# Kernel optimization log

Measured on AMD Instinct MI355X. Metric: run time of the kernel, lower is better.

## Reference

```python
import jax, jax.numpy as jnp
import numpy as np

B, S, D, H, NL, V = 2, 512, 768, 12, 6, 32000
HD = D // H
EPS = 1e-6
# Faithful to original buffer: tril(ones, diagonal=-1) -> True strictly below diagonal,
# and masked_fill sets those to -inf (so each query attends to keys k >= q, as in the source).
MASK = jnp.tril(jnp.ones((S, S), dtype=bool), k=-1)


def setup_inputs() -> dict:
    key = jax.random.key(0)
    ks = jax.random.split(key, 12)
    sc = 0.02
    n = lambda k, shp: jax.random.normal(k, shp, dtype=jnp.float32) * sc
    return {
        "x": jax.random.randint(ks[0], (B, S), 0, V),
        "token_emb": n(ks[1], (V, D)),
        "pos_emb": n(ks[2], (S, D)),
        "norm1_s": jnp.ones((NL, D)), "norm1_b": jnp.zeros((NL, D)),
        "norm2_s": jnp.ones((NL, D)), "norm2_b": jnp.zeros((NL, D)),
        "wq": n(ks[3], (NL, D, D)), "wk": n(ks[4], (NL, D, D)), "wv": n(ks[5], (NL, D, D)),
        "wo": n(ks[6], (NL, D, D)), "bo": jnp.zeros((NL, D)),
        "w1": n(ks[7], (NL, D, 4 * D)), "b1": jnp.zeros((NL, 4 * D)),
        "w2": n(ks[8], (NL, 4 * D, D)), "b2": jnp.zeros((NL, D)),
        "final_s": jnp.ones((D,)), "final_b": jnp.zeros((D,)),
        "head_w": n(ks[9], (D, V)), "head_b": jnp.zeros((V,)),
    }


def _norm(x, s, b):
    # DummyNorm: torch.std default is unbiased (ddof=1); divides by (std + eps), no sqrt(var+eps)
    mean = x.mean(axis=-1, keepdims=True)
    std = jnp.std(x, axis=-1, ddof=1, keepdims=True)
    return s * (x - mean) / (std + EPS) + b


def _gelu(x):
    return 0.5 * x * (1.0 + jnp.tanh(jnp.sqrt(2.0 / jnp.pi) * (x + 0.044715 * x ** 3)))


def _block(x, p):
    wq, wk, wv, wo, bo, w1, b1, w2, b2, n1s, n1b, n2s, n2b = p
    res = x
    h = _norm(x, n1s, n1b)
    q = jnp.einsum("bsd,de->bse", h, wq).reshape(B, S, H, HD)
    k = jnp.einsum("bsd,de->bse", h, wk).reshape(B, S, H, HD)
    v = jnp.einsum("bsd,de->bse", h, wv).reshape(B, S, H, HD)
    scores = jnp.einsum("bqhd,bkhd->bhqk", q, k)
    scores = jnp.where(MASK, -jnp.inf, scores)
    w = jax.nn.softmax(scores / jnp.float32(HD) ** 0.5, axis=-1)  # dropout: eval mode (identity)
    ctx = jnp.einsum("bhqk,bkhd->bqhd", w, v).reshape(B, S, D)
    x = res + (ctx @ wo + bo)
    res = x
    h = _norm(x, n2s, n2b)
    x = res + (_gelu(h @ w1 + b1) @ w2 + b2)
    return x


def reference(x, token_emb, pos_emb, norm1_s, norm1_b, norm2_s, norm2_b,
              wq, wk, wv, wo, bo, w1, b1, w2, b2, final_s, final_b, head_w, head_b):
    h = token_emb[x] + pos_emb[None, :S, :]  # dropout is identity in eval
    params = (wq, wk, wv, wo, bo, w1, b1, w2, b2, norm1_s, norm1_b, norm2_s, norm2_b)
    h = jax.lax.scan(lambda c, p: (_block(c, p), None), h, params)[0]
    h = _norm(h, final_s, final_b)
    return h @ head_w + head_b  # [B, S, V]
```

## Files before the change

### kernel.cpp

```cpp
#include <hip/hip_runtime.h>
#include <math.h>

#define BDIM 2
#define SEQ 512
#define DMODEL 768
#define NHEAD 12
#define HDIM 64
#define NLAYER 6
#define VOCAB 32000
#define MROWS (BDIM*SEQ)
#define EPSV 1e-6f

typedef unsigned short u16;
typedef unsigned int u32;
typedef __bf16 bf16x8 __attribute__((ext_vector_type(8)));
typedef float f32x4 __attribute__((ext_vector_type(4)));

__device__ __forceinline__ u16 f2bf(float f) {
    union { float f; u32 u; } v; v.f = f;
    u32 r = v.u + 0x7fffu + ((v.u >> 16) & 1u);
    return (u16)(r >> 16);
}
__device__ __forceinline__ float bf2f(u16 b) {
    union { u32 u; float f; } v; v.u = ((u32)b) << 16;
    return v.f;
}

__device__ __forceinline__ void gload16(const u16* g, u16* l) {
    __builtin_amdgcn_global_load_lds(
        (const __attribute__((address_space(1))) unsigned int*)g,
        (__attribute__((address_space(3))) unsigned int*)l,
        16, 0, 0);
}

__global__ void embed_kernel(const int* __restrict__ x, const float* __restrict__ tok,
                             const float* __restrict__ pos, float* __restrict__ h) {
    int i = blockIdx.x * blockDim.x + threadIdx.x;
    if (i >= MROWS * DMODEL) return;
    int bs = i / DMODEL, d = i - bs * DMODEL;
    int s = bs & (SEQ - 1);
    h[i] = tok[(size_t)x[bs] * DMODEL + d] + pos[(size_t)s * DMODEL + d];
}

__global__ __launch_bounds__(256) void transpose_conv(const float* __restrict__ in, u16* __restrict__ out,
                                                      int K, int N, long in_bs, long out_bs) {
    __shared__ float t[32][33];
    int b = blockIdx.z;
    int n0 = blockIdx.x * 32, k0 = blockIdx.y * 32;
    int tx = threadIdx.x, ty = threadIdx.y;
    const float* ip = in + (size_t)b * in_bs;
    #pragma unroll
    for (int i = 0; i < 4; ++i)
        t[ty + 8 * i][tx] = ip[(size_t)(k0 + ty + 8 * i) * N + n0 + tx];
    __syncthreads();
    u16* op = out + (size_t)b * out_bs;
    #pragma unroll
    for (int i = 0; i < 4; ++i)
        op[(size_t)(n0 + ty + 8 * i) * K + k0 + tx] = f2bf(t[tx][ty + 8 * i]);
}

template<bool OUTBF>
__global__ __launch_bounds__(256) void norm_kernel(const float* __restrict__ in,
                                                   const float* __restrict__ scale,
                                                   const float* __restrict__ bias,
                                                   void* __restrict__ outp) {
    int row = blockIdx.x;
    const float* xr = in + (size_t)row * DMODEL;
    int t = threadIdx.x;
    float v0 = xr[t], v1 = xr[t + 256], v2 = xr[t + 512];

    float s = v0 + v1 + v2;
    for (int o = 32; o > 0; o >>= 1) s += __shfl_down(s, o);
    __shared__ float red1[4];
    __shared__ float red2[4];
    int wid = t >> 6, lane = t & 63;
    if (lane == 0) red1[wid] = s;
    __syncthreads();
    float mean = (red1[0] + red1[1] + red1[2] + red1[3]) * (1.0f / DMODEL);

    float d0 = v0 - mean, d1 = v1 - mean, d2 = v2 - mean;
    float ss = d0 * d0 + d1 * d1 + d2 * d2;
    for (int o = 32; o > 0; o >>= 1) ss += __shfl_xor(ss, o);
    if (lane == 0) red2[wid] = ss;
    __syncthreads();
    float var = (red2[0] + red2[1] + red2[2] + red2[3]) * (1.0f / (DMODEL - 1));
    float inv = 1.0f / (sqrtf(var) + EPSV);

    size_t o0 = (size_t)row * DMODEL + t;
    float r0 = scale[t] * d0 * inv + bias[t];
    float r1 = scale[t + 256] * d1 * inv + bias[t + 256];
    float r2 = scale[t + 512] * d2 * inv + bias[t + 512];
    if (OUTBF) {
        u16* out = (u16*)outp;
        out[o0] = f2bf(r0); out[o0 + 256] = f2bf(r1); out[o0 + 512] = f2bf(r2);
    } else {
        float* out = (float*)outp;
        out[o0] = r0; out[o0 + 256] = r1; out[o0 + 512] = r2;
    }
}


template<bool OUTBF, bool BIAS, bool RES, bool GELU, bool SWZ>
__global__ __launch_bounds__(256) void gemm_bf16(const u16* __restrict__ A,
                                                 const u16* __restrict__ Wt,
                                                 const float* __restrict__ bias,
                                                 const float* __restrict__ res,
                                                 void* __restrict__ Cout,
                                                 int M, int N, int K) {
    __shared__ u16 Alds[2][128 * 64];
    __shared__ u16 Blds[2][128 * 64];
    int tid = threadIdx.x;
    int lane = tid & 63;
    int wid = tid >> 6;
    int l15 = lane & 15, lk = lane >> 4;
    int wm = (wid >> 1) * 64, wn = (wid & 1) * 64;
    int bm, bn;
    if (SWZ) {
        int id = blockIdx.x;
        int xcd = id & 7, j = id >> 3;
        int g = xcd * ((int)gridDim.x >> 3) + j;
        int mb = M >> 7;
        bn = (g / mb) * 128;
        bm = (g % mb) * 128;
    } else {
        bm = blockIdx.y * 128; bn = blockIdx.x * 128;
    }

    f32x4 acc[4][4];
    #pragma unroll
    for (int i = 0; i < 4; ++i)
        #pragma unroll
        for (int j = 0; j < 4; ++j) { f32x4 z = {0.f, 0.f, 0.f, 0.f}; acc[i][j] = z; }

    int lr  = lane >> 3;
    int lc8 = (lane & 7) ^ lr;
    const u16* gA = A  + (size_t)(bm + lr) * K + lc8 * 8;
    const u16* gB = Wt + (size_t)(bn + lr) * K + lc8 * 8;
    int wrow = wid * 32;

    auto STAGE = [&](int buf, int k0) {
        #pragma unroll
        for (int i = 0; i < 4; ++i) {
            int rb = wrow + i * 8;
            gload16(gA + (size_t)rb * K + k0, &Alds[buf][rb * 64]);
            gload16(gB + (size_t)rb * K + k0, &Blds[buf][rb * 64]);
        }
    };

    STAGE(0, 0);
    __syncthreads();
    int nt = K >> 6;
    int cur = 0;
    for (int t = 0; t < nt; ++t) {
        if (t + 1 < nt) STAGE(cur ^ 1, (t + 1) << 6);

        #pragma unroll
        for (int s = 0; s < 2; ++s) {
            bf16x8 af[4], bfv[4];
            #pragma unroll
            for (int mi = 0; mi < 4; ++mi) {
                int R = wm + mi * 16 + l15;
                af[mi] = *(const bf16x8*)&Alds[cur][R * 64 + (((s * 4 + lk) ^ (R & 7)) << 3)];
            }
            #pragma unroll
            for (int ni = 0; ni < 4; ++ni) {
                int R = wn + ni * 16 + l15;
                bfv[ni] = *(const bf16x8*)&Blds[cur][R * 64 + (((s * 4 + lk) ^ (R & 7)) << 3)];
            }
            #pragma unroll
            for (int mi = 0; mi < 4; ++mi)
                #pragma unroll
                for (int ni = 0; ni < 4; ++ni)
                    acc[mi][ni] = __builtin_amdgcn_mfma_f32_16x16x32_bf16(af[mi], bfv[ni], acc[mi][ni], 0, 0, 0);
        }
        __syncthreads();
        cur ^= 1;
    }

    #pragma unroll
    for (int mi = 0; mi < 4; ++mi) {
        int row0 = bm + wm + mi * 16 + lk * 4;
        #pragma unroll
        for (int ni = 0; ni < 4; ++ni) {
            int col = bn + wn + ni * 16 + l15;
            float bv = BIAS ? bias[col] : 0.0f;
            #pragma unroll
            for (int rr = 0; rr < 4; ++rr) {
                int row = row0 + rr;
                float v = acc[mi][ni][rr] + bv;
                if (GELU) {
                    float xg = v;
                    v = 0.5f * xg * (1.0f + tanhf(0.7978845608028654f * (xg + 0.044715f * xg * xg * xg)));
                }
                if (RES) v += res[(size_t)row * N + col];
                if (OUTBF) ((u16*)Cout)[(size_t)row * N + col] = f2bf(v);
                else       ((float*)Cout)[(size_t)row * N + col] = v;
            }
        }
    }
}

template<bool OUTBF, bool BIAS, bool RES, bool GELU, int BM, int BN>
__global__ __launch_bounds__(256) void gemm_sm(const u16* __restrict__ A,
                                               const u16* __restrict__ Wt,
                                               const float* __restrict__ bias,
                                               const float* __restrict__ res,
                                               void* __restrict__ Cout,
                                               int M, int N, int K) {
    __shared__ u16 Alds[2][BM * 64];
    __shared__ u16 Blds[2][BN * 64];
    int tid = threadIdx.x;
    int lane = tid & 63;
    int wid = tid >> 6;
    int l15 = lane & 15, lk = lane >> 4;
    int wr = wid >> 1, wc = wid & 1;
    int bm = blockIdx.y * BM, bn = blockIdx.x * BN;
    constexpr int MI = BM / 32;
    constexpr int NI = BN / 32;

    f32x4 acc[MI][NI];
    #pragma unroll
    for (int i = 0; i < MI; ++i)
        #pragma unroll
        for (int j = 0; j < NI; ++j) { f32x4 z = {0.f, 0.f, 0.f, 0.f}; acc[i][j] = z; }

    int lr  = lane >> 3;
    int lc8 = (lane & 7) ^ lr;
    const u16* gA = A  + (size_t)(bm + lr) * K + lc8 * 8;
    const u16* gB = Wt + (size_t)(bn + lr) * K + lc8 * 8;

    auto STAGE = [&](int buf, int k0) {
        #pragma unroll
        for (int i = 0; i < MI; ++i) {
            int rb = wid * (BM / 4) + i * 8;
            gload16(gA + (size_t)rb * K + k0, &Alds[buf][rb * 64]);
        }
        #pragma unroll
        for (int i = 0; i < NI; ++i) {
            int rb = wid * (BN / 4) + i * 8;
            gload16(gB + (size_t)rb * K + k0, &Blds[buf][rb * 64]);
        }
    };

    STAGE(0, 0);
    __syncthreads();
    int nt = K >> 6;
    int cur = 0;
    for (int t = 0; t < nt; ++t) {
        if (t + 1 < nt) STAGE(cur ^ 1, (t + 1) << 6);

        #pragma unroll
        for (int s = 0; s < 2; ++s) {
            bf16x8 af[MI], bfv[NI];
            #pragma unroll
            for (int mi = 0; mi < MI; ++mi) {
                int R = wr * (BM / 2) + mi * 16 + l15;
                af[mi] = *(const bf16x8*)&Alds[cur][R * 64 + (((s * 4 + lk) ^ (R & 7)) << 3)];
            }
            #pragma unroll
            for (int ni = 0; ni < NI; ++ni) {
                int R = wc * (BN / 2) + ni * 16 + l15;
                bfv[ni] = *(const bf16x8*)&Blds[cur][R * 64 + (((s * 4 + lk) ^ (R & 7)) << 3)];
            }
            #pragma unroll
            for (int mi = 0; mi < MI; ++mi)
                #pragma unroll
                for (int ni = 0; ni < NI; ++ni)
                    acc[mi][ni] = __builtin_amdgcn_mfma_f32_16x16x32_bf16(af[mi], bfv[ni], acc[mi][ni], 0, 0, 0);
        }
        __syncthreads();
        cur ^= 1;
    }

    #pragma unroll
    for (int mi = 0; mi < MI; ++mi) {
        int row0 = bm + wr * (BM / 2) + mi * 16 + lk * 4;
        #pragma unroll
        for (int ni = 0; ni < NI; ++ni) {
            int col = bn + wc * (BN / 2) + ni * 16 + l15;
            float bv = BIAS ? bias[col] : 0.0f;
            #pragma unroll
            for (int rr = 0; rr < 4; ++rr) {
                int row = row0 + rr;
                float v = acc[mi][ni][rr] + bv;
                if (GELU) {
                    float xg = v;
                    v = 0.5f * xg * (1.0f + tanhf(0.7978845608028654f * (xg + 0.044715f * xg * xg * xg)));
                }
                if (RES) v += res[(size_t)row * N + col];
                if (OUTBF) ((u16*)Cout)[(size_t)row * N + col] = f2bf(v);
                else       ((float*)Cout)[(size_t)row * N + col] = v;
            }
        }
    }
}

__device__ __forceinline__ float bcast_q(float f0, float f1, float f2, float f3, int l15) {
    int src = (l15 >> 2) * 16;
    float a = __shfl(f0, src, 64);
    float b = __shfl(f1, src, 64);
    float c = __shfl(f2, src, 64);
    float d = __shfl(f3, src, 64);
    int r = l15 & 3;
    return r == 0 ? a : (r == 1 ? b : (r == 2 ? c : d));
}

__global__ __launch_bounds__(256) void attn_mfma(const u16* __restrict__ qkv, u16* __restrict__ ctx) {
    int qt = blockIdx.x;
    int bh = blockIdx.y;
    int b = bh / NHEAD, h = bh % NHEAD;
    int tid = threadIdx.x;
    int w = tid >> 6, lane = tid & 63;
    int l15 = lane & 15, lk = lane >> 4;

    __shared__ u16 Klds[64][72];
    __shared__ u16 Vt[64][72];
    __shared__ u16 Plds[4][16][72];

    int q0 = qt * 64;
    const u16* qbase = qkv + (size_t)(b * SEQ + q0 + w * 16 + l15) * 2304 + h * HDIM;
    bf16x8 qf0 = *(const bf16x8*)(qbase + lk * 8);
    bf16x8 qf1 = *(const bf16x8*)(qbase + 32 + lk * 8);

    f32x4 acc_o[4];
    #pragma unroll
    for (int i = 0; i < 4; ++i) { f32x4 z = {0.f,0.f,0.f,0.f}; acc_o[i] = z; }
    float m_run[4] = {-INFINITY, -INFINITY, -INFINITY, -INFINITY};
    float l_run[4] = {0.f, 0.f, 0.f, 0.f};

    int srow = tid >> 2, sc = (tid & 3) * 16;
    int vcol = srow ^ ((sc >> 4) << 4);
    const u16* kg = qkv + (size_t)(b * SEQ) * 2304 + 768  + h * HDIM;
    const u16* vg = qkv + (size_t)(b * SEQ) * 2304 + 1536 + h * HDIM;

    for (int kt = qt; kt < SEQ / 64; ++kt) {
        int kk0 = kt * 64;
        const u16* kp = kg + (size_t)(kk0 + srow) * 2304 + sc;
        const u16* vp = vg + (size_t)(kk0 + srow) * 2304 + sc;
        uint4 kv0 = *(const uint4*)kp, kv1 = *(const uint4*)(kp + 8);
        uint4 vv0 = *(const uint4*)vp, vv1 = *(const uint4*)(vp + 8);
        __syncthreads();
        *(uint4*)&Klds[srow][sc]     = kv0;
        *(uint4*)&Klds[srow][sc + 8] = kv1;
        {
            const u16* vs = (const u16*)&vv0;
            #pragma unroll
            for (int i = 0; i < 8; ++i) Vt[sc + i][vcol] = vs[i];
            const u16* vs1 = (const u16*)&vv1;
            #pragma unroll
            for (int i = 0; i < 8; ++i) Vt[sc + 8 + i][vcol] = vs1[i];
        }
        __syncthreads();

        f32x4 accs[4];
        #pragma unroll
        for (int kb = 0; kb < 4; ++kb) { f32x4 z = {0.f,0.f,0.f,0.f}; accs[kb] = z; }
        __builtin_amdgcn_s_setprio(1);
        #pragma unroll
        for (int kb = 0; kb < 4; ++kb) {
            bf16x8 kf0 = *(const bf16x8*)&Klds[kb * 16 + l15][lk * 8];
            bf16x8 kf1 = *(const bf16x8*)&Klds[kb * 16 + l15][32 + lk * 8];
            accs[kb] = __builtin_amdgcn_mfma_f32_16x16x32_bf16(qf0, kf0, accs[kb], 0, 0, 0);
            accs[kb] = __builtin_amdgcn_mfma_f32_16x16x32_bf16(qf1, kf1, accs[kb], 0, 0, 0);
        }
        __builtin_amdgcn_s_setprio(0);

        bool diag = (kt == qt);
        float s[4][4];
        #pragma unroll
        for (int kb = 0; kb < 4; ++kb)
            #pragma unroll
            for (int r = 0; r < 4; ++r) {
                float v = accs[kb][r] * 0.125f;
                if (diag && (kk0 + kb * 16 + l15) < (q0 + w * 16 + lk * 4 + r)) v = -INFINITY;
                s[kb][r] = v;
            }
        float fac[4];
        #pragma unroll
        for (int r = 0; r < 4; ++r) {
            float mx = fmaxf(fmaxf(s[0][r], s[1][r]), fmaxf(s[2][r], s[3][r]));
            #pragma unroll
            for (int o = 8; o >= 1; o >>= 1) mx = fmaxf(mx, __shfl_xor(mx, o, 64));
            float mn = fmaxf(m_run[r], mx);
            fac[r] = expf(m_run[r] - mn);
            m_run[r] = mn;
        }
        u16 pb[4][4];
        #pragma unroll
        for (int r = 0; r < 4; ++r) {
            float rs = 0.f;
            #pragma unroll
            for (int kb = 0; kb < 4; ++kb) {
                float p = expf(s[kb][r] - m_run[r]);
                pb[kb][r] = f2bf(p);
                rs += p;
            }
            #pragma unroll
            for (int o = 8; o >= 1; o >>= 1) rs += __shfl_xor(rs, o, 64);
            l_run[r] = l_run[r] * fac[r] + rs;
        }
        #pragma unroll
        for (int kb = 0; kb < 4; ++kb)
            #pragma unroll
            for (int r = 0; r < 4; ++r)
                Plds[w][lk * 4 + r][kb * 16 + l15] = pb[kb][r];
        float fq = bcast_q(fac[0], fac[1], fac[2], fac[3], l15);
        #pragma unroll
        for (int db = 0; db < 4; ++db)
            #pragma unroll
            for (int r = 0; r < 4; ++r) acc_o[db][r] *= fq;
        __syncthreads();

        __builtin_amdgcn_s_setprio(1);
        #pragma unroll
        for (int ks = 0; ks < 2; ++ks) {
            bf16x8 pf = *(const bf16x8*)&Plds[w][l15][ks * 32 + lk * 8];
            #pragma unroll
            for (int db = 0; db < 4; ++db) {
                bf16x8 vf = *(const bf16x8*)&Vt[db * 16 + l15][(ks * 32 + lk * 8) ^ (db << 4)];
                acc_o[db] = __builtin_amdgcn_mfma_f32_16x16x32_bf16(vf, pf, acc_o[db], 0, 0, 0);
            }
        }
        __builtin_amdgcn_s_setprio(0);
    }

    float invq;
    {
        float i0 = 1.0f / l_run[0], i1 = 1.0f / l_run[1], i2 = 1.0f / l_run[2], i3 = 1.0f / l_run[3];
        invq = bcast_q(i0, i1, i2, i3, l15);
    }
    u16* cp = ctx + (size_t)(b * SEQ + q0 + w * 16 + l15) * DMODEL + h * HDIM;
    #pragma unroll
    for (int db = 0; db < 4; ++db) {
        ushort4 st;
        st.x = f2bf(acc_o[db][0] * invq);
        st.y = f2bf(acc_o[db][1] * invq);
        st.z = f2bf(acc_o[db][2] * invq);
        st.w = f2bf(acc_o[db][3] * invq);
        *(ushort4*)(cp + db * 16 + lk * 4) = st;
    }
}

template<bool BIAS, bool RES, bool GELU>
__global__ __launch_bounds__(256) void gemm_f32(const float* __restrict__ A, const float* __restrict__ W,
                                                const float* __restrict__ bias, const float* __restrict__ res,
                                                float* __restrict__ C, int M, int N, int K) {
    const int BM = 64, BN = 64, BK = 16;
    __shared__ float sA[BK][BM + 4];
    __shared__ float sB[BK][BN + 4];
    int tid = threadIdx.x;
    int tx = tid & 15, ty = tid >> 4;
    int bm = blockIdx.y * BM, bn = blockIdx.x * BN;
    float acc[4][4] = {};
    const float* Ab = A + (size_t)bm * K;
    const float* Wb = W + bn;
    for (int k0 = 0; k0 < K; k0 += BK) {
        {
            int rr = tid >> 2, c = (tid & 3) * 4;
            float4 va = *(const float4*)(Ab + (size_t)rr * K + k0 + c);
            sA[c + 0][rr] = va.x; sA[c + 1][rr] = va.y; sA[c + 2][rr] = va.z; sA[c + 3][rr] = va.w;
        }
        {
            int rr = tid >> 4, c = (tid & 15) * 4;
            float4 vb = *(const float4*)(Wb + (size_t)(k0 + rr) * N + c);
            *(float4*)(&sB[rr][c]) = vb;
        }
        __syncthreads();
        #pragma unroll
        for (int kk = 0; kk < BK; ++kk) {
            float4 a4 = *(const float4*)(&sA[kk][ty * 4]);
            float4 b4 = *(const float4*)(&sB[kk][tx * 4]);
            float a[4] = {a4.x, a4.y, a4.z, a4.w};
            float b[4] = {b4.x, b4.y, b4.z, b4.w};
            #pragma unroll
            for (int i = 0; i < 4; ++i)
                #pragma unroll
                for (int j = 0; j < 4; ++j) acc[i][j] += a[i] * b[j];
        }
        __syncthreads();
    }
    #pragma unroll
    for (int i = 0; i < 4; ++i) {
        int row = bm + ty * 4 + i;
        #pragma unroll
        for (int j = 0; j < 4; ++j) {
            int col = bn + tx * 4 + j;
            float v = acc[i][j];
            if (BIAS) v += bias[col];
            if (GELU) { float xg = v; v = 0.5f * xg * (1.0f + tanhf(0.7978845608028654f * (xg + 0.044715f * xg * xg * xg))); }
            if (RES) v += res[(size_t)row * N + col];
            C[(size_t)row * N + col] = v;
        }
    }
}

__global__ __launch_bounds__(256) void attn_f32(const float* __restrict__ q, const float* __restrict__ k,
                                                const float* __restrict__ v, float* __restrict__ ctx) {
    int blk = blockIdx.x;
    int qi = blk & (SEQ - 1);
    int tmp = blk >> 9;
    int h = tmp % NHEAD;
    int b = tmp / NHEAD;
    int tid = threadIdx.x;
    __shared__ float qv[HDIM];
    __shared__ float p[SEQ];
    __shared__ float rmax[4];
    __shared__ float rsum[4];
    __shared__ float part[4][HDIM];
    const float* qptr = q + ((size_t)(b * SEQ + qi) * DMODEL + h * HDIM);
    if (tid < HDIM) qv[tid] = qptr[tid];
    __syncthreads();
    float sc[2];
    #pragma unroll
    for (int c = 0; c < 2; ++c) {
        int kk = tid + c * 256;
        const float* kptr = k + ((size_t)(b * SEQ + kk) * DMODEL + h * HDIM);
        float dot = 0.0f;
        #pragma unroll
        for (int d = 0; d < HDIM; ++d) dot += qv[d] * kptr[d];
        sc[c] = (kk >= qi) ? dot * 0.125f : -INFINITY;
    }
    int wid = tid >> 6, lane = tid & 63;
    float m = fmaxf(sc[0], sc[1]);
    for (int o = 32; o > 0; o >>= 1) m = fmaxf(m, __shfl_down(m, o));
    if (lane == 0) rmax[wid] = m;
    __syncthreads();
    m = fmaxf(fmaxf(rmax[0], rmax[1]), fmaxf(rmax[2], rmax[3]));
    float e0 = expf(sc[0] - m);
    float e1 = expf(sc[1] - m);
    p[tid] = e0; p[tid + 256] = e1;
    float sum = e0 + e1;
    for (int o = 32; o > 0; o >>= 1) sum += __shfl_down(sum, o);
    if (lane == 0) rsum[wid] = sum;
    __syncthreads();
    float inv = 1.0f / (rsum[0] + rsum[1] + rsum[2] + rsum[3]);
    int d = tid & 63, ch = tid >> 6;
    float accv = 0.0f;
    const float* vbase = v + ((size_t)b * SEQ * DMODEL + h * HDIM + d);
    for (int kk = ch * 128; kk < (ch + 1) * 128; ++kk) accv += p[kk] * vbase[(size_t)kk * DMODEL];
    part[ch][d] = accv;
    __syncthreads();
    if (tid < HDIM) {
        float rv = (part[0][tid] + part[1][tid] + part[2][tid] + part[3][tid]) * inv;
        ctx[((size_t)(b * SEQ + qi) * DMODEL + h * HDIM + tid)] = rv;
    }
}

extern "C" void kernel_launch(void* const* d_in, const int* in_sizes, int n_in,
                              void* d_out, int out_size, void* d_ws, size_t ws_size,
                              hipStream_t stream) {
    const int*   x   = (const int*)d_in[0];
    const float* tok = (const float*)d_in[1];
    const float* pos = (const float*)d_in[2];
    const float* n1s = (const float*)d_in[3];
    const float* n1b = (const float*)d_in[4];
    const float* n2s = (const float*)d_in[5];
    const float* n2b = (const float*)d_in[6];
    const float* wq  = (const float*)d_in[7];
    const float* wk  = (const float*)d_in[8];
    const float* wv  = (const float*)d_in[9];
    const float* wo  = (const float*)d_in[10];
    const float* bo  = (const float*)d_in[11];
    const float* w1  = (const float*)d_in[12];
    const float* b1  = (const float*)d_in[13];
    const float* w2  = (const float*)d_in[14];
    const float* b2  = (const float*)d_in[15];
    const float* fs  = (const float*)d_in[16];
    const float* fb  = (const float*)d_in[17];
    const float* hw  = (const float*)d_in[18];
    const float* hb  = (const float*)d_in[19];
    float* out = (float*)d_out;

    const size_t szWtQKV = (size_t)NLAYER * 2304 * 768 * 2;
    const size_t szWtO   = (size_t)NLAYER * 768 * 768 * 2;
    const size_t szWt1   = (size_t)NLAYER * 3072 * 768 * 2;
    const size_t szWt2   = (size_t)NLAYER * 768 * 3072 * 2;
    const size_t szWtH   = (size_t)VOCAB * 768 * 2;
    const size_t szH     = (size_t)MROWS * DMODEL * 4;
    const size_t szHN    = (size_t)MROWS * DMODEL * 2;
    const size_t szQKV   = (size_t)MROWS * 2304 * 2;
    const size_t szCTX   = (size_t)MROWS * DMODEL * 2;
    const size_t szFF    = (size_t)MROWS * 3072 * 2;
    const size_t NEED = szWtQKV + szWtO + szWt1 + szWt2 + szWtH + szH + szHN + szQKV + szCTX + szFF;

    if (ws_size >= NEED) {
        char* p = (char*)d_ws;
        u16* WtQKV = (u16*)p; p += szWtQKV;
        u16* WtO   = (u16*)p; p += szWtO;
        u16* Wt1   = (u16*)p; p += szWt1;
        u16* Wt2   = (u16*)p; p += szWt2;
        u16* WtH   = (u16*)p; p += szWtH;
        float* h   = (float*)p; p += szH;
        u16* hn    = (u16*)p; p += szHN;
        u16* qkv   = (u16*)p; p += szQKV;
        u16* ctx   = (u16*)p; p += szCTX;
        u16* ff    = (u16*)p; p += szFF;

        dim3 tb(32, 8);
        transpose_conv<<<dim3(24, 24, NLAYER), tb, 0, stream>>>(wq, WtQKV + 0 * 768 * 768, 768, 768, 768 * 768, 2304 * 768);
        transpose_conv<<<dim3(24, 24, NLAYER), tb, 0, stream>>>(wk, WtQKV + 1 * 768 * 768, 768, 768, 768 * 768, 2304 * 768);
        transpose_conv<<<dim3(24, 24, NLAYER), tb, 0, stream>>>(wv, WtQKV + 2 * 768 * 768, 768, 768, 768 * 768, 2304 * 768);
        transpose_conv<<<dim3(24, 24, NLAYER), tb, 0, stream>>>(wo, WtO, 768, 768, 768 * 768, 768 * 768);
        transpose_conv<<<dim3(96, 24, NLAYER), tb, 0, stream>>>(w1, Wt1, 768, 3072, 768 * 3072, 3072 * 768);
        transpose_conv<<<dim3(24, 96, NLAYER), tb, 0, stream>>>(w2, Wt2, 3072, 768, 3072 * 768, 768 * 3072);
        transpose_conv<<<dim3(1000, 24, 1), tb, 0, stream>>>(hw, WtH, 768, VOCAB, 0, 0);

        embed_kernel<<<(MROWS * DMODEL + 255) / 256, 256, 0, stream>>>(x, tok, pos, h);

        for (int l = 0; l < NLAYER; ++l) {
            const u16* wtqkv = WtQKV + (size_t)l * 2304 * 768;
            const u16* wto   = WtO   + (size_t)l * 768 * 768;
            const u16* wt1   = Wt1   + (size_t)l * 3072 * 768;
            const u16* wt2   = Wt2   + (size_t)l * 768 * 3072;

            norm_kernel<true><<<MROWS, 256, 0, stream>>>(h, n1s + l * DMODEL, n1b + l * DMODEL, hn);
            gemm_sm<true,false,false,false,64,64><<<dim3(36, 16), 256, 0, stream>>>(hn, wtqkv, nullptr, nullptr, qkv, MROWS, 2304, 768);
            attn_mfma<<<dim3(8, 24), 256, 0, stream>>>(qkv, ctx);
            gemm_sm<false,true,true,false,32,64><<<dim3(12, 32), 256, 0, stream>>>(ctx, wto, bo + l * DMODEL, h, h, MROWS, 768, 768);
            norm_kernel<true><<<MROWS, 256, 0, stream>>>(h, n2s + l * DMODEL, n2b + l * DMODEL, hn);
            gemm_sm<true,true,false,true,64,64><<<dim3(48, 16), 256, 0, stream>>>(hn, wt1, b1 + (size_t)l * 3072, nullptr, ff, MROWS, 3072, 768);
            gemm_sm<false,true,true,false,32,64><<<dim3(12, 32), 256, 0, stream>>>(ff, wt2, b2 + l * DMODEL, h, h, MROWS, 768, 3072);
        }
        norm_kernel<true><<<MROWS, 256, 0, stream>>>(h, fs, fb, hn);
        gemm_bf16<false,true,false,false,true><<<2000, 256, 0, stream>>>(hn, WtH, hb, nullptr, out, MROWS, VOCAB, 768);
        return;
    }

    float* ws  = (float*)d_ws;
    float* h   = ws;
    float* hnf = h   + (size_t)MROWS * DMODEL;
    float* qb  = hnf + (size_t)MROWS * DMODEL;
    float* kb  = qb  + (size_t)MROWS * DMODEL;
    float* vb  = kb  + (size_t)MROWS * DMODEL;
    float* ctxf= vb  + (size_t)MROWS * DMODEL;
    float* fff = ctxf+ (size_t)MROWS * DMODEL;

    embed_kernel<<<(MROWS * DMODEL + 255) / 256, 256, 0, stream>>>(x, tok, pos, h);
    dim3 g768(DMODEL / 64, MROWS / 64);
    dim3 g3072(4 * DMODEL / 64, MROWS / 64);
    dim3 gV(VOCAB / 64, MROWS / 64);
    for (int l = 0; l < NLAYER; ++l) {
        size_t wOff  = (size_t)l * DMODEL * DMODEL;
        size_t w1Off = (size_t)l * DMODEL * 4 * DMODEL;
        norm_kernel<false><<<MROWS, 256, 0, stream>>>(h, n1s + l * DMODEL, n1b + l * DMODEL, hnf);
        gemm_f32<false,false,false><<<g768, 256, 0, stream>>>(hnf, wq + wOff, nullptr, nullptr, qb, MROWS, DMODEL, DMODEL);
        gemm_f32<false,false,false><<<g768, 256, 0, stream>>>(hnf, wk + wOff, nullptr, nullptr, kb, MROWS, DMODEL, DMODEL);
        gemm_f32<false,false,false><<<g768, 256, 0, stream>>>(hnf, wv + wOff, nullptr, nullptr, vb, MROWS, DMODEL, DMODEL);
        attn_f32<<<BDIM * NHEAD * SEQ, 256, 0, stream>>>(qb, kb, vb, ctxf);
        gemm_f32<true,true,false><<<g768, 256, 0, stream>>>(ctxf, wo + wOff, bo + l * DMODEL, h, h, MROWS, DMODEL, DMODEL);
        norm_kernel<false><<<MROWS, 256, 0, stream>>>(h, n2s + l * DMODEL, n2b + l * DMODEL, hnf);
        gemm_f32<true,false,true><<<g3072, 256, 0, stream>>>(hnf, w1 + w1Off, b1 + (size_t)l * 4 * DMODEL, nullptr, fff, MROWS, 4 * DMODEL, DMODEL);
        gemm_f32<true,true,false><<<g768, 256, 0, stream>>>(fff, w2 + w1Off, b2 + l * DMODEL, h, h, MROWS, DMODEL, 4 * DMODEL);
    }
    norm_kernel<false><<<MROWS, 256, 0, stream>>>(h, fs, fb, hnf);
    gemm_f32<true,false,false><<<gV, 256, 0, stream>>>(hnf, hw, hb, nullptr, out, MROWS, VOCAB, DMODEL);
}
```

Baseline: 802.9 us.

## Remap GEMM and attention blocks across XCDs and widen weight transpose tiles

The GEMM and attention kernels now use a 1D grid, and the block index is remapped so that consecutive logical tiles land on the same XCD (id&7). Blocks sharing weight columns or the same heads then reuse that XCD's L2 cache. The weight transpose/convert kernel moves from 32x32 to 64x64 tiles, with float4 loads and ushort4 stores to cut memory transactions. The remapping assumes grid sizes are multiples of 8 and that hardware dispatches blocks round-robin across XCDs. The 64x65 float LDS tile reads columns with a stride that may cause bank conflicts.

Measured after the change: 798.0 us. Within noise of the previous version (-0.6%).

```diff
diff --git a/kernel.cpp b/kernel.cpp
--- a/kernel.cpp
+++ b/kernel.cpp
@@ -44,19 +44,30 @@
 
 __global__ __launch_bounds__(256) void transpose_conv(const float* __restrict__ in, u16* __restrict__ out,
                                                       int K, int N, long in_bs, long out_bs) {
-    __shared__ float t[32][33];
+    __shared__ float t[64][65];
     int b = blockIdx.z;
-    int n0 = blockIdx.x * 32, k0 = blockIdx.y * 32;
-    int tx = threadIdx.x, ty = threadIdx.y;
+    int n0 = blockIdx.x * 64, k0 = blockIdx.y * 64;
+    int tid = threadIdx.x;
     const float* ip = in + (size_t)b * in_bs;
-    #pragma unroll
-    for (int i = 0; i < 4; ++i)
-        t[ty + 8 * i][tx] = ip[(size_t)(k0 + ty + 8 * i) * N + n0 + tx];
+    int kr = tid >> 4, nc = (tid & 15) * 4;
+    #pragma unroll
+    for (int i = 0; i < 4; ++i) {
+        float4 v = *(const float4*)(ip + (size_t)(k0 + kr + i * 16) * N + n0 + nc);
+        t[kr + i * 16][nc] = v.x; t[kr + i * 16][nc + 1] = v.y;
+        t[kr + i * 16][nc + 2] = v.z; t[kr + i * 16][nc + 3] = v.w;
+    }
     __syncthreads();
     u16* op = out + (size_t)b * out_bs;
-    #pragma unroll
-    for (int i = 0; i < 4; ++i)
-        op[(size_t)(n0 + ty + 8 * i) * K + k0 + tx] = f2bf(t[tx][ty + 8 * i]);
+    int nr = tid >> 4, kc = (tid & 15) * 4;
+    #pragma unroll
+    for (int i = 0; i < 4; ++i) {
+        ushort4 s;
+        s.x = f2bf(t[kc + 0][nr + i * 16]);
+        s.y = f2bf(t[kc + 1][nr + i * 16]);
+        s.z = f2bf(t[kc + 2][nr + i * 16]);
+        s.w = f2bf(t[kc + 3][nr + i * 16]);
+        *(ushort4*)(op + (size_t)(n0 + nr + i * 16) * K + k0 + kc) = s;
+    }
 }
 
 template<bool OUTBF>
@@ -214,7 +225,12 @@
     int wid = tid >> 6;
     int l15 = lane & 15, lk = lane >> 4;
     int wr = wid >> 1, wc = wid & 1;
-    int bm = blockIdx.y * BM, bn = blockIdx.x * BN;
+    int id = blockIdx.x;
+    int xcd = id & 7, j = id >> 3;
+    int g = xcd * ((int)gridDim.x >> 3) + j;
+    int mb = M / BM;
+    int bn = (g / mb) * BN;
+    int bm = (g % mb) * BM;
     constexpr int MI = BM / 32;
     constexpr int NI = BN / 32;
 
@@ -222,7 +238,7 @@
     #pragma unroll
     for (int i = 0; i < MI; ++i)
         #pragma unroll
-        for (int j = 0; j < NI; ++j) { f32x4 z = {0.f, 0.f, 0.f, 0.f}; acc[i][j] = z; }
+        for (int j2 = 0; j2 < NI; ++j2) { f32x4 z = {0.f, 0.f, 0.f, 0.f}; acc[i][j2] = z; }
 
     int lr  = lane >> 3;
     int lc8 = (lane & 7) ^ lr;
@@ -306,8 +322,10 @@
 }
 
 __global__ __launch_bounds__(256) void attn_mfma(const u16* __restrict__ qkv, u16* __restrict__ ctx) {
-    int qt = blockIdx.x;
-    int bh = blockIdx.y;
+    int id = blockIdx.x;
+    int slot = id & 7, r0_ = id >> 3;
+    int qt = r0_ & 7;
+    int bh = (r0_ >> 3) * 8 + slot;
     int b = bh / NHEAD, h = bh % NHEAD;
     int tid = threadIdx.x;
     int w = tid >> 6, lane = tid & 63;
@@ -596,14 +614,13 @@
         u16* ctx   = (u16*)p; p += szCTX;
         u16* ff    = (u16*)p; p += szFF;
 
-        dim3 tb(32, 8);
-        transpose_conv<<<dim3(24, 24, NLAYER), tb, 0, stream>>>(wq, WtQKV + 0 * 768 * 768, 768, 768, 768 * 768, 2304 * 768);
-        transpose_conv<<<dim3(24, 24, NLAYER), tb, 0, stream>>>(wk, WtQKV + 1 * 768 * 768, 768, 768, 768 * 768, 2304 * 768);
-        transpose_conv<<<dim3(24, 24, NLAYER), tb, 0, stream>>>(wv, WtQKV + 2 * 768 * 768, 768, 768, 768 * 768, 2304 * 768);
-        transpose_conv<<<dim3(24, 24, NLAYER), tb, 0, stream>>>(wo, WtO, 768, 768, 768 * 768, 768 * 768);
-        transpose_conv<<<dim3(96, 24, NLAYER), tb, 0, stream>>>(w1, Wt1, 768, 3072, 768 * 3072, 3072 * 768);
-        transpose_conv<<<dim3(24, 96, NLAYER), tb, 0, stream>>>(w2, Wt2, 3072, 768, 3072 * 768, 768 * 3072);
-        transpose_conv<<<dim3(1000, 24, 1), tb, 0, stream>>>(hw, WtH, 768, VOCAB, 0, 0);
+        transpose_conv<<<dim3(12, 12, NLAYER), 256, 0, stream>>>(wq, WtQKV + 0 * 768 * 768, 768, 768, 768 * 768, 2304 * 768);
+        transpose_conv<<<dim3(12, 12, NLAYER), 256, 0, stream>>>(wk, WtQKV + 1 * 768 * 768, 768, 768, 768 * 768, 2304 * 768);
+        transpose_conv<<<dim3(12, 12, NLAYER), 256, 0, stream>>>(wv, WtQKV + 2 * 768 * 768, 768, 768, 768 * 768, 2304 * 768);
+        transpose_conv<<<dim3(12, 12, NLAYER), 256, 0, stream>>>(wo, WtO, 768, 768, 768 * 768, 768 * 768);
+        transpose_conv<<<dim3(48, 12, NLAYER), 256, 0, stream>>>(w1, Wt1, 768, 3072, 768 * 3072, 3072 * 768);
+        transpose_conv<<<dim3(12, 48, NLAYER), 256, 0, stream>>>(w2, Wt2, 3072, 768, 3072 * 768, 768 * 3072);
+        transpose_conv<<<dim3(500, 12, 1), 256, 0, stream>>>(hw, WtH, 768, VOCAB, 0, 0);
 
         embed_kernel<<<(MROWS * DMODEL + 255) / 256, 256, 0, stream>>>(x, tok, pos, h);
 
@@ -614,12 +631,12 @@
             const u16* wt2   = Wt2   + (size_t)l * 768 * 3072;
 
             norm_kernel<true><<<MROWS, 256, 0, stream>>>(h, n1s + l * DMODEL, n1b + l * DMODEL, hn);
-            gemm_sm<true,false,false,false,64,64><<<dim3(36, 16), 256, 0, stream>>>(hn, wtqkv, nullptr, nullptr, qkv, MROWS, 2304, 768);
-            attn_mfma<<<dim3(8, 24), 256, 0, stream>>>(qkv, ctx);
-            gemm_sm<false,true,true,false,32,64><<<dim3(12, 32), 256, 0, stream>>>(ctx, wto, bo + l * DMODEL, h, h, MROWS, 768, 768);
+            gemm_sm<true,false,false,false,64,64><<<576, 256, 0, stream>>>(hn, wtqkv, nullptr, nullptr, qkv, MROWS, 2304, 768);
+            attn_mfma<<<192, 256, 0, stream>>>(qkv, ctx);
+            gemm_sm<false,true,true,false,32,64><<<384, 256, 0, stream>>>(ctx, wto, bo + l * DMODEL, h, h, MROWS, 768, 768);
             norm_kernel<true><<<MROWS, 256, 0, stream>>>(h, n2s + l * DMODEL, n2b + l * DMODEL, hn);
-            gemm_sm<true,true,false,true,64,64><<<dim3(48, 16), 256, 0, stream>>>(hn, wt1, b1 + (size_t)l * 3072, nullptr, ff, MROWS, 3072, 768);
-            gemm_sm<false,true,true,false,32,64><<<dim3(12, 32), 256, 0, stream>>>(ff, wt2, b2 + l * DMODEL, h, h, MROWS, 768, 3072);
+            gemm_sm<true,true,false,true,64,64><<<768, 256, 0, stream>>>(hn, wt1, b1 + (size_t)l * 3072, nullptr, ff, MROWS, 3072, 768);
+            gemm_sm<false,true,true,false,32,64><<<384, 256, 0, stream>>>(ff, wt2, b2 + l * DMODEL, h, h, MROWS, 768, 3072);
         }
         norm_kernel<true><<<MROWS, 256, 0, stream>>>(h, fs, fb, hn);
         gemm_bf16<false,true,false,false,true><<<2000, 256, 0, stream>>>(hn, WtH, hb, nullptr, out, MROWS, VOCAB, 768);
```
